# Performance work log

Hardware: AMD Instinct MI355X
Metric: run time of the kernel (lower is better)

The kernel has to match this reference:

```python
import jax, jax.numpy as jnp
import numpy as np

D_MODEL = 1024
HEADS = 16
D_K = D_MODEL // HEADS
SCALE = 1.0 / np.sqrt(D_K)


def setup_inputs() -> dict:
    key = jax.random.key(0)
    ks = jax.random.split(key, 12)
    B, S = 4, 2048
    std = 1.0 / np.sqrt(D_MODEL)
    inp = {
        "query": jax.random.normal(ks[0], (B, S, D_MODEL), jnp.float32),
        "key": jax.random.normal(ks[1], (B, S, D_MODEL), jnp.float32),
        "value": jax.random.normal(ks[2], (B, S, D_MODEL), jnp.float32),
        # projection weights stored [in, out] (transpose of torch Linear)
        "Wq": jax.random.normal(ks[3], (D_MODEL, D_MODEL), jnp.float32) * std,
        "bq": jax.random.normal(ks[4], (D_MODEL,), jnp.float32) * std,
        "Wk": jax.random.normal(ks[5], (D_MODEL, D_MODEL), jnp.float32) * std,
        "bk": jax.random.normal(ks[6], (D_MODEL,), jnp.float32) * std,
        "Wv": jax.random.normal(ks[7], (D_MODEL, D_MODEL), jnp.float32) * std,
        "bv": jax.random.normal(ks[8], (D_MODEL,), jnp.float32) * std,
        "Wo": jax.random.normal(ks[9], (D_MODEL, D_MODEL), jnp.float32) * std,
        "bo": jax.random.normal(ks[10], (D_MODEL,), jnp.float32) * std,
    }
    return inp


def _proj(x, W, b):
    # [B,S,D] -> [B,S,H,Dk]
    B, S, _ = x.shape
    return (x @ W + b).reshape(B, S, HEADS, D_K)


def reference(query, key, value, Wq, bq, Wk, bk, Wv, bv, Wo, bo):
    B, S, _ = query.shape
    Q = _proj(query, Wq, bq)
    K = _proj(key, Wk, bk)
    V = _proj(value, Wv, bv)
    scores = jnp.einsum('bihd,bjhd->bijh', Q, K) * SCALE
    # FAITHFUL to original: nn.Softmax(dim=1) normalizes over the QUERY axis i
    attn = jax.nn.softmax(scores, axis=1)
    # dropout is identity at inference
    x = jnp.einsum('bijh,bjhd->bihd', attn, V).reshape(B, S, D_MODEL)
    return x @ Wo + bo
```

## Files before the change

kernel.cpp:

```cpp
#include <hip/hip_runtime.h>


#define B_   4
#define S_   2048
#define D_   1024
#define H_   16
#define DK_  64
#define BH_  64
#define SC2_    0.18033688f

typedef __bf16 bf16x2 __attribute__((ext_vector_type(2)));
typedef __bf16 bf16x4 __attribute__((ext_vector_type(4)));
typedef __bf16 bf16x8 __attribute__((ext_vector_type(8)));
typedef float  f32x4  __attribute__((ext_vector_type(4)));
typedef unsigned int u32;

#define MFMA16(a,b,c) __builtin_amdgcn_mfma_f32_16x16x32_bf16((a),(b),(c),0,0,0)

__device__ __forceinline__ bf16x8 ld8(const __bf16* p){ return *(const bf16x8*)p; }

__device__ __forceinline__ void gll16(const __bf16* g, __bf16* l) {
    __builtin_amdgcn_global_load_lds(
        (const __attribute__((address_space(1))) u32*)g,
        (__attribute__((address_space(3))) u32*)l, 16, 0, 0);
}

__global__ __launch_bounds__(256) void wtrans3(
    const float* __restrict__ W0, const float* __restrict__ W1,
    const float* __restrict__ W2, __bf16* __restrict__ Wt)
{
    __shared__ __align__(16) __bf16 Ls[64][80];
    const int t = threadIdx.x;
    const int k0 = blockIdx.x * 64, n0 = blockIdx.y * 64, z = blockIdx.z;
    const float* W = (z == 0) ? W0 : ((z == 1) ? W1 : W2);
    __bf16* out = Wt + (size_t)z * D_ * D_;

#pragma unroll
    for (int p = 0; p < 4; ++p) {
        int id = p*256 + t;
        int k = id >> 4, nq = id & 15;
        f32x4 v = *(const f32x4*)&W[(size_t)(k0 + k)*D_ + n0 + nq*4];
#pragma unroll
        for (int u = 0; u < 4; ++u) Ls[nq*4 + u][k] = (__bf16)v[u];
    }
    __syncthreads();
#pragma unroll
    for (int p = 0; p < 2; ++p) {
        int id = p*256 + t;
        int n = id >> 3, c = id & 7;
        *(bf16x8*)&out[(size_t)(n0 + n)*D_ + k0 + c*8] =
            *(const bf16x8*)&Ls[n][c*8];
    }
}

template<int ABF16, int MODE>
__device__ __forceinline__ void gemm_body(
    const void* __restrict__ Ap, const __bf16* __restrict__ Wt,
    const float* __restrict__ bias, void* __restrict__ C,
    float scale, int m0, int n0)
{
    __shared__ __align__(16) __bf16 As[2][128*64];
    __shared__ __align__(16) __bf16 Bs[2][128*64];

    const int t = threadIdx.x, lane = t & 63, w = t >> 6;
    const int wm = w >> 1, wn = w & 1;
    const int fr = lane & 15, fq = lane >> 4;

    const __bf16* Ab = (const __bf16*)Ap;
    const float*  Af = (const float*)Ap;

    f32x4 acc[4][4];
#pragma unroll
    for (int i = 0; i < 4; ++i)
#pragma unroll
        for (int j = 0; j < 4; ++j) acc[i][j] = (f32x4){0.f,0.f,0.f,0.f};

#define STAGE_B(kk, bsel)                                                     \
    _Pragma("unroll")                                                         \
    for (int p = 0; p < 4; ++p) {                                             \
        int idx = p*256 + t;                                                  \
        int n = idx >> 3, l = (idx & 7) ^ (n & 7);                            \
        gll16(&Wt[(size_t)(n0 + n)*D_ + (kk) + l*8],                          \
              &Bs[bsel][(size_t)(p*256 + (t & ~63))*8]);                      \
    }

#define STAGE_A_BF(kk, bsel)                                                  \
    _Pragma("unroll")                                                         \
    for (int p = 0; p < 4; ++p) {                                             \
        int idx = p*256 + t;                                                  \
        int row = idx >> 3, l = (idx & 7) ^ (row & 7);                        \
        gll16(&Ab[(size_t)(m0 + row)*D_ + (kk) + l*8],                        \
              &As[bsel][(size_t)(p*256 + (t & ~63))*8]);                      \
    }

#define LOAD_A_F32(kk, xa)                                                    \
    _Pragma("unroll")                                                         \
    for (int p = 0; p < 4; ++p) {                                             \
        int idx = p*256 + t;                                                  \
        int row = idx >> 3, l = (idx & 7) ^ (row & 7);                        \
        const float* ap = &Af[(size_t)(m0 + row)*D_ + (kk) + l*8];            \
        xa[2*p]   = *(const f32x4*)ap;                                        \
        xa[2*p+1] = *(const f32x4*)(ap + 4);                                  \
    }

#define WRITE_A_F32(xa, bsel)                                                 \
    _Pragma("unroll")                                                         \
    for (int p = 0; p < 4; ++p) {                                             \
        f32x4 x0 = xa[2*p], x1 = xa[2*p+1];                                   \
        bf16x8 v = { (__bf16)x0[0], (__bf16)x0[1], (__bf16)x0[2],             \
                     (__bf16)x0[3], (__bf16)x1[0], (__bf16)x1[1],             \
                     (__bf16)x1[2], (__bf16)x1[3] };                          \
        *(bf16x8*)&As[bsel][(size_t)(p*256 + t)*8] = v;                       \
    }

    if (ABF16) {
        STAGE_A_BF(0, 0)
    } else {
        f32x4 xa[8];
        LOAD_A_F32(0, xa)
        WRITE_A_F32(xa, 0)
    }
    STAGE_B(0, 0)
    __syncthreads();

    for (int kk = 0; kk < D_; kk += 64) {
        const int cur = (kk >> 6) & 1;
        const bool more = (kk + 64) < D_;

        f32x4 xa[8];
        if (more) {
            if (ABF16) {
                STAGE_A_BF(kk + 64, cur ^ 1)
            } else {
                LOAD_A_F32(kk + 64, xa)
            }
            STAGE_B(kk + 64, cur ^ 1)
        }

#pragma unroll
        for (int kh = 0; kh < 2; ++kh) {
            bf16x8 af[4], bfr[4];
#pragma unroll
            for (int mt = 0; mt < 4; ++mt) {
                int row = wm*64 + mt*16 + fr;
                af[mt] = ld8(&As[cur][row*64 + 8*((kh*4 + fq) ^ (row & 7))]);
            }
#pragma unroll
            for (int nt = 0; nt < 4; ++nt) {
                int n = wn*64 + nt*16 + fr;
                bfr[nt] = ld8(&Bs[cur][n*64 + 8*((kh*4 + fq) ^ (n & 7))]);
            }
#pragma unroll
            for (int mt = 0; mt < 4; ++mt)
#pragma unroll
                for (int nt = 0; nt < 4; ++nt)
                    acc[mt][nt] = MFMA16(af[mt], bfr[nt], acc[mt][nt]);
        }

        if (more && !ABF16) {
            WRITE_A_F32(xa, cur ^ 1)
        }
        __syncthreads();
    }
#undef STAGE_B
#undef STAGE_A_BF
#undef LOAD_A_F32
#undef WRITE_A_F32

#pragma unroll
    for (int mt = 0; mt < 4; ++mt)
#pragma unroll
        for (int nt = 0; nt < 4; ++nt) {
            int colg = n0 + wn*64 + nt*16 + fr;
            float bv = bias[colg];
#pragma unroll
            for (int r = 0; r < 4; ++r) {
                int rowg = m0 + wm*64 + mt*16 + fq*4 + r;
                float o = (acc[mt][nt][r] + bv) * scale;
                if (MODE == 0) {
                    ((float*)C)[(size_t)rowg*D_ + colg] = o;
                } else {
                    int b = rowg >> 11, sp = rowg & (S_-1);
                    int h = colg >> 6, dk = colg & 63;
                    ((__bf16*)C)[(((size_t)(b*H_ + h))*S_ + sp)*DK_ + dk] = (__bf16)o;
                }
            }
        }
}

template<int ABF16, int MODE>
__global__ __launch_bounds__(256) void gemm128(
    const void* __restrict__ Ap, const __bf16* __restrict__ Wt,
    const float* __restrict__ bias, void* __restrict__ C, float scale)
{
    const int gid = blockIdx.x;
    gemm_body<ABF16, MODE>(Ap, Wt, bias, C, scale,
                           (gid & 63) * 128, ((gid >> 6) & 7) * 128);
}

__global__ __launch_bounds__(256) void gemm_proj3(
    const float* __restrict__ q, const float* __restrict__ k,
    const float* __restrict__ v, const __bf16* __restrict__ Wt3,
    const float* __restrict__ bq, const float* __restrict__ bk,
    const float* __restrict__ bv,
    __bf16* __restrict__ Qb, __bf16* __restrict__ Kb, __bf16* __restrict__ Vb)
{
    const int gid = blockIdx.x;
    const int z = gid >> 9, inner = gid & 511;
    const float*  A    = (z == 0) ? q  : ((z == 1) ? k  : v);
    const __bf16* Wt   = Wt3 + (size_t)z * D_ * D_;
    const float*  bias = (z == 0) ? bq : ((z == 1) ? bk : bv);
    __bf16*       C    = (z == 0) ? Qb : ((z == 1) ? Kb : Vb);
    const float scale  = (z == 0) ? SC2_ : 1.0f;
    gemm_body<0, 1>(A, Wt, bias, C, scale,
                    (inner & 63) * 128, (inner >> 6) * 128);
}

__global__ __launch_bounds__(256) void colsum_rcp(
    const __bf16* __restrict__ Q, const __bf16* __restrict__ K,
    float* __restrict__ Lg)
{
    __shared__ __align__(16) __bf16 Qs[2][64*64];
    const int t = threadIdx.x, lane = t & 63, w = t >> 6;
    const int fr = lane & 15, fq = lane >> 4;
    const int gid = blockIdx.x;
    const int bh = gid & 63;
    const int jw = (gid >> 6)*128 + w*32;
    const __bf16* Qb = Q + (size_t)bh*S_*DK_;
    const __bf16* Kb = K + (size_t)bh*S_*DK_;

    bf16x8 kh[2][2];
#pragma unroll
    for (int jt = 0; jt < 2; ++jt) {
        const __bf16* kr = &Kb[(size_t)(jw + jt*16 + fr)*DK_];
        kh[jt][0] = ld8(kr + fq*8);
        kh[jt][1] = ld8(kr + 32 + fq*8);
    }

    float accl[2][4] = {};

#pragma unroll
    for (int p = 0; p < 2; ++p) {
        int c = p*256 + t;
        int i = c >> 3, l = (c & 7) ^ (i & 7);
        gll16(&Qb[(size_t)i*DK_ + l*8], &Qs[0][(size_t)(p*256 + (t & ~63))*8]);
    }
    __syncthreads();

    for (int i0 = 0; i0 < S_; i0 += 64) {
        const int cur = (i0 >> 6) & 1;
        if (i0 + 64 < S_) {
#pragma unroll
            for (int p = 0; p < 2; ++p) {
                int c = p*256 + t;
                int i = c >> 3, l = (c & 7) ^ (i & 7);
                gll16(&Qb[(size_t)(i0 + 64 + i)*DK_ + l*8],
                      &Qs[cur ^ 1][(size_t)(p*256 + (t & ~63))*8]);
            }
        }
#pragma unroll
        for (int it = 0; it < 4; ++it) {
            int i = it*16 + fr;
            bf16x8 q0 = ld8(&Qs[cur][i*64 + 8*(fq ^ (i & 7))]);
            bf16x8 q1 = ld8(&Qs[cur][i*64 + 8*((4 + fq) ^ (i & 7))]);
#pragma unroll
            for (int jt = 0; jt < 2; ++jt) {
                f32x4 s = MFMA16(kh[jt][0], q0, ((f32x4){0.f,0.f,0.f,0.f}));
                s = MFMA16(kh[jt][1], q1, s);
#pragma unroll
                for (int r = 0; r < 4; ++r)
                    accl[jt][r] += __builtin_amdgcn_exp2f(s[r]);
            }
        }
        __syncthreads();
    }
#pragma unroll
    for (int jt = 0; jt < 2; ++jt)
#pragma unroll
        for (int r = 0; r < 4; ++r) {
            accl[jt][r] += __shfl_xor(accl[jt][r], 1, 64);
            accl[jt][r] += __shfl_xor(accl[jt][r], 2, 64);
            accl[jt][r] += __shfl_xor(accl[jt][r], 4, 64);
            accl[jt][r] += __shfl_xor(accl[jt][r], 8, 64);
        }
    if (fr == 0) {
#pragma unroll
        for (int jt = 0; jt < 2; ++jt)
#pragma unroll
            for (int r = 0; r < 4; ++r)
                Lg[(size_t)bh*S_ + jw + jt*16 + fq*4 + r] =
                    -__log2f(accl[jt][r]);
    }
}

__global__ __launch_bounds__(512, 4) void attn_pv(
    const __bf16* __restrict__ Q, const __bf16* __restrict__ K,
    const __bf16* __restrict__ V, const float* __restrict__ Lg,
    __bf16* __restrict__ X)
{
    __shared__ __align__(16) __bf16 Ks[2][64*64];
    __shared__ __align__(16) __bf16 Vs[2][64*64];
    __shared__ __align__(16) __bf16 Pl[8][32*64];

    const int t = threadIdx.x, lane = t & 63, w = t >> 6;
    const int fr = lane & 15, fq = lane >> 4;
    const int gid = blockIdx.x;
    const int bh = gid & 63;
    const int iw = (gid >> 6)*256 + w*32;
    const __bf16* Qb = Q + (size_t)bh*S_*DK_;
    const __bf16* Kb = K + (size_t)bh*S_*DK_;
    const __bf16* Vb = V + (size_t)bh*S_*DK_;
    const float*  Rb = Lg + (size_t)bh*S_;

    bf16x8 qf[2][2];
#pragma unroll
    for (int it = 0; it < 2; ++it)
#pragma unroll
        for (int kf = 0; kf < 2; ++kf)
            qf[it][kf] = ld8(&Qb[(size_t)(iw + it*16 + fr)*DK_ + kf*32 + fq*8]);

    const int dq = t & 15, jp = t >> 4;
    const int krow = t >> 3;
    const int kchk = (t & 7) ^ (krow & 7);

    f32x4 acc[2][4];
#pragma unroll
    for (int it = 0; it < 2; ++it)
#pragma unroll
        for (int dt = 0; dt < 4; ++dt) acc[it][dt] = (f32x4){0.f,0.f,0.f,0.f};

    gll16(&Kb[(size_t)krow*DK_ + kchk*8], &Ks[0][(t & ~63)*8]);
    __syncthreads();

    for (int jg = 0; jg < S_; jg += 64) {
        const int cur = (jg >> 6) & 1;

        bf16x4 v0 = *(const bf16x4*)&Vb[(size_t)(jg + 2*jp    )*DK_ + dq*4];
        bf16x4 v1 = *(const bf16x4*)&Vb[(size_t)(jg + 2*jp + 1)*DK_ + dq*4];
        f32x4 lg[4];
#pragma unroll
        for (int jt = 0; jt < 4; ++jt)
            lg[jt] = *(const f32x4*)&Rb[jg + jt*16 + fq*4];
        if (jg + 64 < S_)
            gll16(&Kb[(size_t)(jg + 64 + krow)*DK_ + kchk*8],
                  &Ks[cur ^ 1][(t & ~63)*8]);

#pragma unroll
        for (int jt = 0; jt < 4; ++jt) {
            const __bf16* kb = &Ks[cur][(jt*16 + fr)*64];
            bf16x8 af0 = ld8(kb + ((fq    ) ^ (fr & 7))*8);
            bf16x8 af1 = ld8(kb + ((fq + 4) ^ (fr & 7))*8);
#pragma unroll
            for (int it = 0; it < 2; ++it) {
                f32x4 s = MFMA16(af0, qf[it][0], lg[jt]);
                s = MFMA16(af1, qf[it][1], s);
                bf16x4 pv;
#pragma unroll
                for (int r = 0; r < 4; ++r)
                    pv[r] = (__bf16)__builtin_amdgcn_exp2f(s[r]);
                int il = it*16 + fr;
                *(bf16x4*)&Pl[w][il*64 + (((jt*4 + fq) ^ (2*(fr & 7))))*4] = pv;
            }
        }

#pragma unroll
        for (int u = 0; u < 4; ++u) {
            int d = dq*4 + u;
            int f = (d ^ dq) & 7;
            *(bf16x2*)&Vs[cur][d*64 + (((jp >> 2) ^ f))*8 + (jp & 3)*2] =
                (bf16x2){ v0[u], v1[u] };
        }
        __syncthreads();

        __builtin_amdgcn_s_setprio(1);
#pragma unroll
        for (int kh = 0; kh < 2; ++kh) {
            bf16x8 pa0 = ld8(&Pl[w][(     fr)*64 + (((fq + 4*kh) ^ (fr & 7)))*8]);
            bf16x8 pa1 = ld8(&Pl[w][(16 + fr)*64 + (((fq + 4*kh) ^ (fr & 7)))*8]);
#pragma unroll
            for (int dt = 0; dt < 4; ++dt) {
                int d = dt*16 + fr;
                int f = (d ^ (d >> 2)) & 7;
                bf16x8 vb = ld8(&Vs[cur][d*64 + (((kh*4 + fq) ^ f))*8]);
                acc[0][dt] = MFMA16(pa0, vb, acc[0][dt]);
                acc[1][dt] = MFMA16(pa1, vb, acc[1][dt]);
            }
        }
        __builtin_amdgcn_s_setprio(0);
    }

    const int b = bh >> 4, h = bh & 15;
#pragma unroll
    for (int it = 0; it < 2; ++it)
#pragma unroll
        for (int dt = 0; dt < 4; ++dt)
#pragma unroll
            for (int r = 0; r < 4; ++r) {
                int i = iw + it*16 + fq*4 + r;
                X[((size_t)b*S_ + i)*D_ + h*DK_ + dt*16 + fr] =
                    (__bf16)acc[it][dt][r];
            }
}

extern "C" void kernel_launch(void* const* d_in, const int* in_sizes, int n_in,
                              void* d_out, int out_size, void* d_ws, size_t ws_size,
                              hipStream_t stream)
{
    const float* query = (const float*)d_in[0];
    const float* key   = (const float*)d_in[1];
    const float* value = (const float*)d_in[2];
    const float* Wq = (const float*)d_in[3];  const float* bq = (const float*)d_in[4];
    const float* Wk = (const float*)d_in[5];  const float* bk = (const float*)d_in[6];
    const float* Wv = (const float*)d_in[7];  const float* bv = (const float*)d_in[8];
    const float* Wo = (const float*)d_in[9];  const float* bo = (const float*)d_in[10];

    char* ws = (char*)d_ws;
    char* dob = (char*)d_out;
    const size_t MiB = 1024 * 1024;
    __bf16* Qb = (__bf16*)(ws);
    __bf16* Kb = (__bf16*)(ws + 16 * MiB);
    __bf16* Vb = (__bf16*)(ws + 32 * MiB);
    __bf16* Xb = (__bf16*)(ws + 48 * MiB);
    float*  Lgb = (float*)d_out;
    __bf16* Wt3 = (__bf16*)(dob + 1 * MiB);
    __bf16* WtO = (__bf16*)(ws);

    wtrans3<<<dim3(16,16,3), 256, 0, stream>>>(Wq, Wk, Wv, Wt3);

    gemm_proj3<<<1536, 256, 0, stream>>>(query, key, value, Wt3,
                                         bq, bk, bv, Qb, Kb, Vb);

    colsum_rcp<<<1024, 256, 0, stream>>>(Qb, Kb, Lgb);

    attn_pv<<<512, 512, 0, stream>>>(Qb, Kb, Vb, Lgb, Xb);

    wtrans3<<<dim3(16,16,1), 256, 0, stream>>>(Wo, Wo, Wo, WtO);

    gemm128<1,0><<<512, 256, 0, stream>>>(Xb, WtO, bo, d_out, 1.0f);
}
```

Measured before the change: 382.4 us.

## Single-buffer QKV projection GEMM and halve colsum rows per block

Replaces the QKV projection GEMM body with a single-buffered variant that converts fp32 activations to bf16 while storing them to swizzled LDS. This halves LDS use per block and may raise occupancy, but it gives up double-buffered overlap of loads with MFMA. The column-sum kernel now handles 16 key rows per wave instead of 32 and launches twice as many blocks. That adds parallelism but re-reads Q twice as often.

```diff
diff --git a/kernel.cpp b/kernel.cpp
--- a/kernel.cpp
+++ b/kernel.cpp
@@ -51,6 +51,102 @@
         *(bf16x8*)&out[(size_t)(n0 + n)*D_ + k0 + c*8] =
             *(const bf16x8*)&Ls[n][c*8];
     }
+}
+
+__device__ __forceinline__ void gemm_sb(
+    const float* __restrict__ Af, const __bf16* __restrict__ Wt,
+    const float* __restrict__ bias, __bf16* __restrict__ C,
+    float scale, int m0, int n0)
+{
+    __shared__ __align__(16) __bf16 As1[128*64];
+    __shared__ __align__(16) __bf16 Bs1[128*64];
+
+    const int t = threadIdx.x, lane = t & 63, w = t >> 6;
+    const int wm = w >> 1, wn = w & 1;
+    const int fr = lane & 15, fq = lane >> 4;
+
+    f32x4 acc[4][4];
+#pragma unroll
+    for (int i = 0; i < 4; ++i)
+#pragma unroll
+        for (int j = 0; j < 4; ++j) acc[i][j] = (f32x4){0.f,0.f,0.f,0.f};
+
+    for (int kk = 0; kk < D_; kk += 64) {
+        __syncthreads();
+#pragma unroll
+        for (int p = 0; p < 4; ++p) {
+            int idx = p*256 + t;
+            int n = idx >> 3, l = (idx & 7) ^ (n & 7);
+            gll16(&Wt[(size_t)(n0 + n)*D_ + kk + l*8],
+                  &Bs1[(size_t)(p*256 + (t & ~63))*8]);
+        }
+#pragma unroll
+        for (int p = 0; p < 4; ++p) {
+            int idx = p*256 + t;
+            int row = idx >> 3, l = (idx & 7) ^ (row & 7);
+            const float* ap = &Af[(size_t)(m0 + row)*D_ + kk + l*8];
+            f32x4 x0 = *(const f32x4*)ap;
+            f32x4 x1 = *(const f32x4*)(ap + 4);
+            bf16x8 v = { (__bf16)x0[0], (__bf16)x0[1], (__bf16)x0[2],
+                         (__bf16)x0[3], (__bf16)x1[0], (__bf16)x1[1],
+                         (__bf16)x1[2], (__bf16)x1[3] };
+            *(bf16x8*)&As1[(size_t)idx*8] = v;
+        }
+        __syncthreads();
+
+#pragma unroll
+        for (int kh = 0; kh < 2; ++kh) {
+            bf16x8 af[4], bfr[4];
+#pragma unroll
+            for (int mt = 0; mt < 4; ++mt) {
+                int row = wm*64 + mt*16 + fr;
+                af[mt] = ld8(&As1[row*64 + 8*((kh*4 + fq) ^ (row & 7))]);
+            }
+#pragma unroll
+            for (int nt = 0; nt < 4; ++nt) {
+                int n = wn*64 + nt*16 + fr;
+                bfr[nt] = ld8(&Bs1[n*64 + 8*((kh*4 + fq) ^ (n & 7))]);
+            }
+#pragma unroll
+            for (int mt = 0; mt < 4; ++mt)
+#pragma unroll
+                for (int nt = 0; nt < 4; ++nt)
+                    acc[mt][nt] = MFMA16(af[mt], bfr[nt], acc[mt][nt]);
+        }
+    }
+
+#pragma unroll
+    for (int mt = 0; mt < 4; ++mt)
+#pragma unroll
+        for (int nt = 0; nt < 4; ++nt) {
+            int colg = n0 + wn*64 + nt*16 + fr;
+            float bv = bias[colg];
+#pragma unroll
+            for (int r = 0; r < 4; ++r) {
+                int rowg = m0 + wm*64 + mt*16 + fq*4 + r;
+                float o = (acc[mt][nt][r] + bv) * scale;
+                int b = rowg >> 11, sp = rowg & (S_-1);
+                int h = colg >> 6, dk = colg & 63;
+                C[(((size_t)(b*H_ + h))*S_ + sp)*DK_ + dk] = (__bf16)o;
+            }
+        }
+}
+
+__global__ __launch_bounds__(256) void gemm_proj3(
+    const float* __restrict__ q, const float* __restrict__ k,
+    const float* __restrict__ v, const __bf16* __restrict__ Wt3,
+    const float* __restrict__ bq, const float* __restrict__ bk,
+    const float* __restrict__ bv,
+    __bf16* __restrict__ Qb, __bf16* __restrict__ Kb, __bf16* __restrict__ Vb)
+{
+    const int gid = blockIdx.x;
+    const int z = gid >> 9, inner = gid & 511;
+    const float*  A    = (z == 0) ? q  : ((z == 1) ? k  : v);
+    const __bf16* Wt   = Wt3 + (size_t)z * D_ * D_;
+    const float*  bias = (z == 0) ? bq : ((z == 1) ? bk : bv);
+    __bf16*       C    = (z == 0) ? Qb : ((z == 1) ? Kb : Vb);
+    const float scale  = (z == 0) ? SC2_ : 1.0f;
+    gemm_sb(A, Wt, bias, C, scale, (inner & 63) * 128, (inner >> 6) * 128);
 }
 
 template<int ABF16, int MODE>
@@ -198,24 +294,6 @@
                            (gid & 63) * 128, ((gid >> 6) & 7) * 128);
 }
 
-__global__ __launch_bounds__(256) void gemm_proj3(
-    const float* __restrict__ q, const float* __restrict__ k,
-    const float* __restrict__ v, const __bf16* __restrict__ Wt3,
-    const float* __restrict__ bq, const float* __restrict__ bk,
-    const float* __restrict__ bv,
-    __bf16* __restrict__ Qb, __bf16* __restrict__ Kb, __bf16* __restrict__ Vb)
-{
-    const int gid = blockIdx.x;
-    const int z = gid >> 9, inner = gid & 511;
-    const float*  A    = (z == 0) ? q  : ((z == 1) ? k  : v);
-    const __bf16* Wt   = Wt3 + (size_t)z * D_ * D_;
-    const float*  bias = (z == 0) ? bq : ((z == 1) ? bk : bv);
-    __bf16*       C    = (z == 0) ? Qb : ((z == 1) ? Kb : Vb);
-    const float scale  = (z == 0) ? SC2_ : 1.0f;
-    gemm_body<0, 1>(A, Wt, bias, C, scale,
-                    (inner & 63) * 128, (inner >> 6) * 128);
-}
-
 __global__ __launch_bounds__(256) void colsum_rcp(
     const __bf16* __restrict__ Q, const __bf16* __restrict__ K,
     float* __restrict__ Lg)
@@ -225,19 +303,18 @@
     const int fr = lane & 15, fq = lane >> 4;
     const int gid = blockIdx.x;
     const int bh = gid & 63;
-    const int jw = (gid >> 6)*128 + w*32;
+    const int jw = (gid >> 6)*64 + w*16;
     const __bf16* Qb = Q + (size_t)bh*S_*DK_;
     const __bf16* Kb = K + (size_t)bh*S_*DK_;
 
-    bf16x8 kh[2][2];
-#pragma unroll
-    for (int jt = 0; jt < 2; ++jt) {
-        const __bf16* kr = &Kb[(size_t)(jw + jt*16 + fr)*DK_];
-        kh[jt][0] = ld8(kr + fq*8);
-        kh[jt][1] = ld8(kr + 32 + fq*8);
-    }
-
-    float accl[2][4] = {};
+    bf16x8 kh0, kh1;
+    {
+        const __bf16* kr = &Kb[(size_t)(jw + fr)*DK_];
+        kh0 = ld8(kr + fq*8);
+        kh1 = ld8(kr + 32 + fq*8);
+    }
+
+    float accl[4] = {};
 
 #pragma unroll
     for (int p = 0; p < 2; ++p) {
@@ -263,33 +340,25 @@
             int i = it*16 + fr;
             bf16x8 q0 = ld8(&Qs[cur][i*64 + 8*(fq ^ (i & 7))]);
             bf16x8 q1 = ld8(&Qs[cur][i*64 + 8*((4 + fq) ^ (i & 7))]);
-#pragma unroll
-            for (int jt = 0; jt < 2; ++jt) {
-                f32x4 s = MFMA16(kh[jt][0], q0, ((f32x4){0.f,0.f,0.f,0.f}));
-                s = MFMA16(kh[jt][1], q1, s);
-#pragma unroll
-                for (int r = 0; r < 4; ++r)
-                    accl[jt][r] += __builtin_amdgcn_exp2f(s[r]);
-            }
+            f32x4 s = MFMA16(kh0, q0, ((f32x4){0.f,0.f,0.f,0.f}));
+            s = MFMA16(kh1, q1, s);
+#pragma unroll
+            for (int r = 0; r < 4; ++r)
+                accl[r] += __builtin_amdgcn_exp2f(s[r]);
         }
         __syncthreads();
     }
 #pragma unroll
-    for (int jt = 0; jt < 2; ++jt)
-#pragma unroll
-        for (int r = 0; r < 4; ++r) {
-            accl[jt][r] += __shfl_xor(accl[jt][r], 1, 64);
-            accl[jt][r] += __shfl_xor(accl[jt][r], 2, 64);
-            accl[jt][r] += __shfl_xor(accl[jt][r], 4, 64);
-            accl[jt][r] += __shfl_xor(accl[jt][r], 8, 64);
-        }
+    for (int r = 0; r < 4; ++r) {
+        accl[r] += __shfl_xor(accl[r], 1, 64);
+        accl[r] += __shfl_xor(accl[r], 2, 64);
+        accl[r] += __shfl_xor(accl[r], 4, 64);
+        accl[r] += __shfl_xor(accl[r], 8, 64);
+    }
     if (fr == 0) {
 #pragma unroll
-        for (int jt = 0; jt < 2; ++jt)
-#pragma unroll
-            for (int r = 0; r < 4; ++r)
-                Lg[(size_t)bh*S_ + jw + jt*16 + fq*4 + r] =
-                    -__log2f(accl[jt][r]);
+        for (int r = 0; r < 4; ++r)
+            Lg[(size_t)bh*S_ + jw + fq*4 + r] = -__log2f(accl[r]);
     }
 }
 
@@ -430,7 +499,7 @@
     gemm_proj3<<<1536, 256, 0, stream>>>(query, key, value, Wt3,
                                          bq, bk, bv, Qb, Kb, Vb);
 
-    colsum_rcp<<<1024, 256, 0, stream>>>(Qb, Kb, Lgb);
+    colsum_rcp<<<2048, 256, 0, stream>>>(Qb, Kb, Lgb);
 
     attn_pv<<<512, 512, 0, stream>>>(Qb, Kb, Vb, Lgb, Xb);
 
```

Result: no change. 381.9 us (-0.1%).

## Triple-buffer GEMM with BK=32 and halve colsum per-block work

Applied to the files above, without the earlier changes.

The projection and output GEMMs move from a double-buffered BK=64 loop to a fully unrolled triple-buffered BK=32 pipeline. Prefetches are issued two stages ahead, and waits use a partial vmcnt plus a raw barrier so loads stay in flight across iterations. Separately, the column-sum kernel gives each wave 16 key rows instead of 32 and launches twice as many blocks for more parallelism, at the cost of redundant Q streaming per block. The pipeline relies on hand-tuned vmcnt values matching the number of outstanding loads, which is fragile.

```diff
diff --git a/kernel.cpp b/kernel.cpp
--- a/kernel.cpp
+++ b/kernel.cpp
@@ -25,6 +25,12 @@
         (__attribute__((address_space(3))) u32*)l, 16, 0, 0);
 }
 
+#define PIPE_BAR(N) do {                                                      \
+    asm volatile("s_waitcnt vmcnt(" #N ") lgkmcnt(0)" ::: "memory");          \
+    __builtin_amdgcn_s_barrier();                                             \
+    __builtin_amdgcn_sched_barrier(0);                                        \
+} while (0)
+
 __global__ __launch_bounds__(256) void wtrans3(
     const float* __restrict__ W0, const float* __restrict__ W1,
     const float* __restrict__ W2, __bf16* __restrict__ Wt)
@@ -54,13 +60,13 @@
 }
 
 template<int ABF16, int MODE>
-__device__ __forceinline__ void gemm_body(
+__device__ __forceinline__ void gemm_pipe(
     const void* __restrict__ Ap, const __bf16* __restrict__ Wt,
     const float* __restrict__ bias, void* __restrict__ C,
     float scale, int m0, int n0)
 {
-    __shared__ __align__(16) __bf16 As[2][128*64];
-    __shared__ __align__(16) __bf16 Bs[2][128*64];
+    __shared__ __align__(16) __bf16 As[3][128*32];
+    __shared__ __align__(16) __bf16 Bs[3][128*32];
 
     const int t = threadIdx.x, lane = t & 63, w = t >> 6;
     const int wm = w >> 1, wn = w & 1;
@@ -75,37 +81,37 @@
 #pragma unroll
         for (int j = 0; j < 4; ++j) acc[i][j] = (f32x4){0.f,0.f,0.f,0.f};
 
-#define STAGE_B(kk, bsel)                                                     \
+#define PSTAGE_B(kk, bsel)                                                    \
     _Pragma("unroll")                                                         \
-    for (int p = 0; p < 4; ++p) {                                             \
-        int idx = p*256 + t;                                                  \
-        int n = idx >> 3, l = (idx & 7) ^ (n & 7);                            \
+    for (int p = 0; p < 2; ++p) {                                             \
+        int id = p*256 + t;                                                   \
+        int n = id >> 2, l = (id & 3) ^ (n & 3);                              \
         gll16(&Wt[(size_t)(n0 + n)*D_ + (kk) + l*8],                          \
               &Bs[bsel][(size_t)(p*256 + (t & ~63))*8]);                      \
     }
 
-#define STAGE_A_BF(kk, bsel)                                                  \
+#define PSTAGE_A_BF(kk, bsel)                                                 \
     _Pragma("unroll")                                                         \
-    for (int p = 0; p < 4; ++p) {                                             \
-        int idx = p*256 + t;                                                  \
-        int row = idx >> 3, l = (idx & 7) ^ (row & 7);                        \
+    for (int p = 0; p < 2; ++p) {                                             \
+        int id = p*256 + t;                                                   \
+        int row = id >> 2, l = (id & 3) ^ (row & 3);                          \
         gll16(&Ab[(size_t)(m0 + row)*D_ + (kk) + l*8],                        \
               &As[bsel][(size_t)(p*256 + (t & ~63))*8]);                      \
     }
 
-#define LOAD_A_F32(kk, xa)                                                    \
+#define PLOAD_A(kk, xa)                                                       \
     _Pragma("unroll")                                                         \
-    for (int p = 0; p < 4; ++p) {                                             \
-        int idx = p*256 + t;                                                  \
-        int row = idx >> 3, l = (idx & 7) ^ (row & 7);                        \
+    for (int p = 0; p < 2; ++p) {                                             \
+        int id = p*256 + t;                                                   \
+        int row = id >> 2, l = (id & 3) ^ (row & 3);                          \
         const float* ap = &Af[(size_t)(m0 + row)*D_ + (kk) + l*8];            \
         xa[2*p]   = *(const f32x4*)ap;                                        \
         xa[2*p+1] = *(const f32x4*)(ap + 4);                                  \
     }
 
-#define WRITE_A_F32(xa, bsel)                                                 \
+#define PCVT_WR(xa, bsel)                                                     \
     _Pragma("unroll")                                                         \
-    for (int p = 0; p < 4; ++p) {                                             \
+    for (int p = 0; p < 2; ++p) {                                             \
         f32x4 x0 = xa[2*p], x1 = xa[2*p+1];                                   \
         bf16x8 v = { (__bf16)x0[0], (__bf16)x0[1], (__bf16)x0[2],             \
                      (__bf16)x0[3], (__bf16)x1[0], (__bf16)x1[1],             \
@@ -113,42 +119,51 @@
         *(bf16x8*)&As[bsel][(size_t)(p*256 + t)*8] = v;                       \
     }
 
+    f32x4 xa0[4], xa1[4];
+
     if (ABF16) {
-        STAGE_A_BF(0, 0)
+        PSTAGE_A_BF(0, 0)  PSTAGE_B(0, 0)
+        PSTAGE_A_BF(32, 1) PSTAGE_B(32, 1)
+        PIPE_BAR(4);
     } else {
-        f32x4 xa[8];
-        LOAD_A_F32(0, xa)
-        WRITE_A_F32(xa, 0)
-    }
-    STAGE_B(0, 0)
-    __syncthreads();
-
-    for (int kk = 0; kk < D_; kk += 64) {
-        const int cur = (kk >> 6) & 1;
-        const bool more = (kk + 64) < D_;
-
-        f32x4 xa[8];
-        if (more) {
-            if (ABF16) {
-                STAGE_A_BF(kk + 64, cur ^ 1)
-            } else {
-                LOAD_A_F32(kk + 64, xa)
-            }
-            STAGE_B(kk + 64, cur ^ 1)
-        }
-
-#pragma unroll
-        for (int kh = 0; kh < 2; ++kh) {
+        PSTAGE_B(0, 0)  PLOAD_A(0, xa0)
+        PSTAGE_B(32, 1) PLOAD_A(32, xa1)
+        PCVT_WR(xa0, 0)
+        PIPE_BAR(6);
+    }
+
+#pragma unroll
+    for (int tt = 0; tt < 32; ++tt) {
+        const int cur = tt % 3, nx1 = (tt + 1) % 3, nx2 = (tt + 2) % 3;
+
+        if (ABF16) {
+            if (tt < 30) {
+                PSTAGE_A_BF(32*(tt + 2), nx2)
+                PSTAGE_B(32*(tt + 2), nx2)
+            }
+        } else {
+            if (tt < 30) {
+                PSTAGE_B(32*(tt + 2), nx2)
+                if (tt & 1) { PLOAD_A(32*(tt + 2), xa1) }
+                else        { PLOAD_A(32*(tt + 2), xa0) }
+            }
+            if (tt < 31) {
+                if (tt & 1) { PCVT_WR(xa0, nx1) }
+                else        { PCVT_WR(xa1, nx1) }
+            }
+        }
+
+        {
             bf16x8 af[4], bfr[4];
 #pragma unroll
             for (int mt = 0; mt < 4; ++mt) {
                 int row = wm*64 + mt*16 + fr;
-                af[mt] = ld8(&As[cur][row*64 + 8*((kh*4 + fq) ^ (row & 7))]);
+                af[mt] = ld8(&As[cur][row*32 + 8*(fq ^ (row & 3))]);
             }
 #pragma unroll
             for (int nt = 0; nt < 4; ++nt) {
                 int n = wn*64 + nt*16 + fr;
-                bfr[nt] = ld8(&Bs[cur][n*64 + 8*((kh*4 + fq) ^ (n & 7))]);
+                bfr[nt] = ld8(&Bs[cur][n*32 + 8*(fq ^ (n & 3))]);
             }
 #pragma unroll
             for (int mt = 0; mt < 4; ++mt)
@@ -157,15 +172,12 @@
                     acc[mt][nt] = MFMA16(af[mt], bfr[nt], acc[mt][nt]);
         }
 
-        if (more && !ABF16) {
-            WRITE_A_F32(xa, cur ^ 1)
-        }
-        __syncthreads();
-    }
-#undef STAGE_B
-#undef STAGE_A_BF
-#undef LOAD_A_F32
-#undef WRITE_A_F32
+        if (ABF16) { PIPE_BAR(4); } else { PIPE_BAR(6); }
+    }
+#undef PSTAGE_B
+#undef PSTAGE_A_BF
+#undef PLOAD_A
+#undef PCVT_WR
 
 #pragma unroll
     for (int mt = 0; mt < 4; ++mt)
@@ -194,7 +206,7 @@
     const float* __restrict__ bias, void* __restrict__ C, float scale)
 {
     const int gid = blockIdx.x;
-    gemm_body<ABF16, MODE>(Ap, Wt, bias, C, scale,
+    gemm_pipe<ABF16, MODE>(Ap, Wt, bias, C, scale,
                            (gid & 63) * 128, ((gid >> 6) & 7) * 128);
 }
 
@@ -212,7 +224,7 @@
     const float*  bias = (z == 0) ? bq : ((z == 1) ? bk : bv);
     __bf16*       C    = (z == 0) ? Qb : ((z == 1) ? Kb : Vb);
     const float scale  = (z == 0) ? SC2_ : 1.0f;
-    gemm_body<0, 1>(A, Wt, bias, C, scale,
+    gemm_pipe<0, 1>(A, Wt, bias, C, scale,
                     (inner & 63) * 128, (inner >> 6) * 128);
 }
 
@@ -225,19 +237,18 @@
     const int fr = lane & 15, fq = lane >> 4;
     const int gid = blockIdx.x;
     const int bh = gid & 63;
-    const int jw = (gid >> 6)*128 + w*32;
+    const int jw = (gid >> 6)*64 + w*16;
     const __bf16* Qb = Q + (size_t)bh*S_*DK_;
     const __bf16* Kb = K + (size_t)bh*S_*DK_;
 
-    bf16x8 kh[2][2];
-#pragma unroll
-    for (int jt = 0; jt < 2; ++jt) {
-        const __bf16* kr = &Kb[(size_t)(jw + jt*16 + fr)*DK_];
-        kh[jt][0] = ld8(kr + fq*8);
-        kh[jt][1] = ld8(kr + 32 + fq*8);
-    }
-
-    float accl[2][4] = {};
+    bf16x8 kh0, kh1;
+    {
+        const __bf16* kr = &Kb[(size_t)(jw + fr)*DK_];
+        kh0 = ld8(kr + fq*8);
+        kh1 = ld8(kr + 32 + fq*8);
+    }
+
+    float accl[4] = {};
 
 #pragma unroll
     for (int p = 0; p < 2; ++p) {
@@ -263,33 +274,25 @@
             int i = it*16 + fr;
             bf16x8 q0 = ld8(&Qs[cur][i*64 + 8*(fq ^ (i & 7))]);
             bf16x8 q1 = ld8(&Qs[cur][i*64 + 8*((4 + fq) ^ (i & 7))]);
-#pragma unroll
-            for (int jt = 0; jt < 2; ++jt) {
-                f32x4 s = MFMA16(kh[jt][0], q0, ((f32x4){0.f,0.f,0.f,0.f}));
-                s = MFMA16(kh[jt][1], q1, s);
-#pragma unroll
-                for (int r = 0; r < 4; ++r)
-                    accl[jt][r] += __builtin_amdgcn_exp2f(s[r]);
-            }
+            f32x4 s = MFMA16(kh0, q0, ((f32x4){0.f,0.f,0.f,0.f}));
+            s = MFMA16(kh1, q1, s);
+#pragma unroll
+            for (int r = 0; r < 4; ++r)
+                accl[r] += __builtin_amdgcn_exp2f(s[r]);
         }
         __syncthreads();
     }
 #pragma unroll
-    for (int jt = 0; jt < 2; ++jt)
-#pragma unroll
-        for (int r = 0; r < 4; ++r) {
-            accl[jt][r] += __shfl_xor(accl[jt][r], 1, 64);
-            accl[jt][r] += __shfl_xor(accl[jt][r], 2, 64);
-            accl[jt][r] += __shfl_xor(accl[jt][r], 4, 64);
-            accl[jt][r] += __shfl_xor(accl[jt][r], 8, 64);
-        }
+    for (int r = 0; r < 4; ++r) {
+        accl[r] += __shfl_xor(accl[r], 1, 64);
+        accl[r] += __shfl_xor(accl[r], 2, 64);
+        accl[r] += __shfl_xor(accl[r], 4, 64);
+        accl[r] += __shfl_xor(accl[r], 8, 64);
+    }
     if (fr == 0) {
 #pragma unroll
-        for (int jt = 0; jt < 2; ++jt)
-#pragma unroll
-            for (int r = 0; r < 4; ++r)
-                Lg[(size_t)bh*S_ + jw + jt*16 + fq*4 + r] =
-                    -__log2f(accl[jt][r]);
+        for (int r = 0; r < 4; ++r)
+            Lg[(size_t)bh*S_ + jw + fq*4 + r] = -__log2f(accl[r]);
     }
 }
 
@@ -430,7 +433,7 @@
     gemm_proj3<<<1536, 256, 0, stream>>>(query, key, value, Wt3,
                                          bq, bk, bv, Qb, Kb, Vb);
 
-    colsum_rcp<<<1024, 256, 0, stream>>>(Qb, Kb, Lgb);
+    colsum_rcp<<<2048, 256, 0, stream>>>(Qb, Kb, Lgb);
 
     attn_pv<<<512, 512, 0, stream>>>(Qb, Kb, Vb, Lgb, Xb);
 
```

New measurement: 385.5 us. No clear change (+0.8%).
